# Kernel tuning notes

Measured on AMD Instinct MI355X. Metric: run time of the kernel, lower is better.

Reference implementation:

```python
import jax, jax.numpy as jnp
import numpy as np

WS = (8, 8)          # window_size
HEADS = 8
DH = 64              # dim_head
SHIFT = (4, 4)
SCALE = DH ** -0.5


def setup_inputs() -> dict:
    key = jax.random.key(0)
    ks = jax.random.split(key, 5)
    dim = 64
    inner = HEADS * DH  # 512
    b, h, w = 4, 192, 192
    x = jax.random.normal(ks[0], (b, h, w, dim), dtype=jnp.float32)
    Wq = jax.random.normal(ks[1], (dim, inner), dtype=jnp.float32) * (dim ** -0.5)
    Wkv = jax.random.normal(ks[2], (dim, 2 * inner), dtype=jnp.float32) * (dim ** -0.5)
    Wo = jax.random.normal(ks[3], (inner, dim), dtype=jnp.float32) * (inner ** -0.5)
    bo = jnp.zeros((dim,), dtype=jnp.float32)
    seq_l = WS[0] * WS[1]
    pos_emb = jax.random.normal(ks[4], (1, HEADS, seq_l, seq_l), dtype=jnp.float32)
    return {"x": x, "Wq": Wq, "Wkv": Wkv, "Wo": Wo, "bo": bo, "pos_emb": pos_emb}


def reference(x, Wq, Wkv, Wo, bo, pos_emb):
    b, h, w, c = x.shape
    L = WS[0] * WS[1]  # 64 tokens per window
    if SHIFT[0] > 0:
        x = jnp.roll(x, shift=(-SHIFT[0], -SHIFT[1]), axis=(1, 2))
    # NOTE: original uses a raw .view() here (row-major reshape), NOT an 8x8
    # window partition. Replicate exactly.
    nw = b * (h // WS[0]) * (w // WS[1])
    x_inp = x.reshape(nw, L, c)                      # [nw, 64, c]
    q = x_inp @ Wq                                   # [nw, 64, inner]
    kv = x_inp @ Wkv
    k, v = jnp.split(kv, 2, axis=-1)
    # original: raw view (nw, L, inner) -> (nw, heads, L, dh) (not a transpose)
    q = q.reshape(nw, HEADS, L, DH) * SCALE
    k = k.reshape(nw, HEADS, L, DH)
    v = v.reshape(nw, HEADS, L, DH)
    sim = jnp.einsum('bhid,bhjd->bhij', q, k) + pos_emb
    attn = jax.nn.softmax(sim, axis=-1)
    out = jnp.einsum('bhij,bhjd->bhid', attn, v)     # [nw, heads, 64, dh]
    # original: raw view back to (nw, L, inner)
    out = out.reshape(nw, L, HEADS * DH)
    out = out @ Wo + bo                              # [nw, 64, c]
    out = out.reshape(b, h, w, c)
    if SHIFT[0] > 0:
        out = jnp.roll(out, shift=(SHIFT[0], SHIFT[1]), axis=(1, 2))
    return out
```

## Files before the change

### kernel.cpp

```cpp
#include <hip/hip_runtime.h>
#include <stdint.h>

typedef __attribute__((ext_vector_type(8))) short bf16x8;
typedef __attribute__((ext_vector_type(4))) short s16x4;
typedef __attribute__((ext_vector_type(4))) float f32x4;

#define THREADS 256
constexpr int NWIN = 2304;

constexpr int WCATT_E = 0;
constexpr int WOT_E   = 98304;
constexpr int POS_E   = 131072;
constexpr size_t WS_NEED = 327680;

__device__ __forceinline__ short f2bf(float f) {
  uint32_t u = __builtin_bit_cast(uint32_t, f);
  u += 0x7fffu + ((u >> 16) & 1u);
  return (short)(u >> 16);
}
__device__ __forceinline__ float bf2f(short s) {
  uint32_t u = ((uint32_t)(uint16_t)s) << 16;
  return __builtin_bit_cast(float, u);
}
__device__ __forceinline__ int swz(int row, int h) {
  return ((((row ^ (row >> 2) ^ (row >> 3)) & 7) ^ h) << 4);
}

__global__ void wmsa_prep(const float* __restrict__ Wq, const float* __restrict__ Wkv,
                          const float* __restrict__ Wo, const float* __restrict__ pos,
                          short* __restrict__ ws) {
  int idx = blockIdx.x * 256 + threadIdx.x;
  if (idx < 32768) {
    int n = idx & 511, k = idx >> 9;
    ws[WCATT_E + n * 64 + k] = f2bf(Wq[k * 512 + n] * 0.125f);
  } else if (idx < 98304) {
    int j = idx - 32768;
    int nkv = j & 1023, k = j >> 10;
    ws[WCATT_E + (512 + nkv) * 64 + k] = f2bf(Wkv[k * 1024 + nkv]);
  } else if (idx < 131072) {
    int j = idx - 98304;
    int n = j & 63, k = j >> 6;
    ws[WOT_E + n * 512 + k] = f2bf(Wo[k * 64 + n]);
  } else if (idx < 163840) {
    int j = idx - 131072;
    ws[POS_E + j] = f2bf(pos[j]);
  }
}

__global__ __launch_bounds__(THREADS, 2)
void wmsa_mfma(const float* __restrict__ x, const float* __restrict__ bo,
               const short* __restrict__ ws, float* __restrict__ out) {
  __shared__ __align__(16) char lds[65536];
  const int tid = threadIdx.x;
  const int wv = tid >> 6;
  const int l  = tid & 63;
  const int lr = l & 15;
  const int lg = l >> 4;

  const int bid = blockIdx.x;
  const int p   = bid >> 2;
  const int hp  = bid & 3;

  const float* xrow[2];
  float* orow[2];
  int ww0a[2];
  #pragma unroll
  for (int win = 0; win < 2; ++win) {
    int w   = 2 * p + win;
    int t0  = w * 64;
    int bb  = t0 / 36864;
    int rem = t0 % 36864;
    int hh  = rem / 192;
    ww0a[win] = rem % 192;
    int src_h = (hh + 4) % 192;
    xrow[win] = x + (size_t)(bb * 192 + src_h) * 12288;
    orow[win] = out + (size_t)(bb * 192 + src_h) * 12288;
  }

  bf16x8 xa[2][2];
  #pragma unroll
  for (int win = 0; win < 2; ++win) {
    int tok = 16 * hp + lr;
    int sw = ww0a[win] + tok + 4; if (sw >= 192) sw -= 192;
    const float* xp = xrow[win] + sw * 64;
    #pragma unroll
    for (int ks = 0; ks < 2; ++ks) {
      float4 a = *(const float4*)(xp + ks * 32 + lg * 8);
      float4 b = *(const float4*)(xp + ks * 32 + lg * 8 + 4);
      bf16x8 v;
      v[0] = f2bf(a.x); v[1] = f2bf(a.y); v[2] = f2bf(a.z); v[3] = f2bf(a.w);
      v[4] = f2bf(b.x); v[5] = f2bf(b.y); v[6] = f2bf(b.z); v[7] = f2bf(b.w);
      xa[win][ks] = v;
    }
  }

  #pragma unroll 4
  for (int t = 0; t < 16; ++t) {
    int nt = wv + 4 * t;
    int nload = nt * 16 + lr;
    bf16x8 b0 = *(const bf16x8*)(ws + WCATT_E + nload * 64 + lg * 8);
    bf16x8 b1 = *(const bf16x8*)(ws + WCATT_E + nload * 64 + 32 + lg * 8);
    const bool isQ = (t < 8);
    int i  = (lr & 7) * 8 + (t & 7);
    int h2 = lr >> 3;
    int d0 = wv * 16 + lg * 4;
    int off = (isQ ? 0 : 16384) + h2 * 8192 + i * 128 + ((d0 * 2) ^ swz(i, h2));
    #pragma unroll
    for (int win = 0; win < 2; ++win) {
      f32x4 acc = {0.f, 0.f, 0.f, 0.f};
      acc = __builtin_amdgcn_mfma_f32_16x16x32_bf16(b0, xa[win][0], acc, 0, 0, 0);
      acc = __builtin_amdgcn_mfma_f32_16x16x32_bf16(b1, xa[win][1], acc, 0, 0, 0);
      s16x4 pk;
      #pragma unroll
      for (int r = 0; r < 4; ++r) pk[r] = f2bf(acc[r]);
      *(s16x4*)(lds + win * 32768 + off) = pk;
    }
  }

  f32x4 vacc[2][8];
  #pragma unroll
  for (int tv = 0; tv < 8; ++tv) {
    int nload = (64 + wv + 4 * tv) * 16 + lr;
    bf16x8 b0 = *(const bf16x8*)(ws + WCATT_E + nload * 64 + lg * 8);
    bf16x8 b1 = *(const bf16x8*)(ws + WCATT_E + nload * 64 + 32 + lg * 8);
    #pragma unroll
    for (int win = 0; win < 2; ++win) {
      f32x4 acc = {0.f, 0.f, 0.f, 0.f};
      acc = __builtin_amdgcn_mfma_f32_16x16x32_bf16(xa[win][0], b0, acc, 0, 0, 0);
      acc = __builtin_amdgcn_mfma_f32_16x16x32_bf16(xa[win][1], b1, acc, 0, 0, 0);
      vacc[win][tv] = acc;
    }
  }
  __syncthreads();

  const int hl = wv >> 1;
  const int ih = wv & 1;
  const int hglob = 2 * hp + hl;

  s16x4 posr[2][4];
  #pragma unroll
  for (int it = 0; it < 2; ++it) {
    int i = (ih * 2 + it) * 16 + lr;
    const short* pp = ws + POS_E + hglob * 4096 + i * 64;
    #pragma unroll
    for (int jt = 0; jt < 4; ++jt)
      posr[it][jt] = *(const s16x4*)(pp + jt * 16 + lg * 4);
  }

  #pragma unroll
  for (int win = 0; win < 2; ++win) {
    char* ldw = lds + win * 32768;
    f32x4 s[2][4];
    #pragma unroll
    for (int it = 0; it < 2; ++it)
      #pragma unroll
      for (int jt = 0; jt < 4; ++jt) s[it][jt] = (f32x4){0.f, 0.f, 0.f, 0.f};

    #pragma unroll
    for (int ks = 0; ks < 2; ++ks) {
      bf16x8 kb[4], qa[2];
      #pragma unroll
      for (int jt = 0; jt < 4; ++jt) {
        int j = jt * 16 + lr;
        kb[jt] = *(const bf16x8*)(ldw + 16384 + hl * 8192 + j * 128 + ((ks * 64 + lg * 16) ^ swz(j, hl)));
      }
      #pragma unroll
      for (int it = 0; it < 2; ++it) {
        int i = (ih * 2 + it) * 16 + lr;
        qa[it] = *(const bf16x8*)(ldw + hl * 8192 + i * 128 + ((ks * 64 + lg * 16) ^ swz(i, hl)));
      }
      __builtin_amdgcn_s_setprio(1);
      #pragma unroll
      for (int it = 0; it < 2; ++it)
        #pragma unroll
        for (int jt = 0; jt < 4; ++jt)
          s[it][jt] = __builtin_amdgcn_mfma_f32_16x16x32_bf16(kb[jt], qa[it], s[it][jt], 0, 0, 0);
      __builtin_amdgcn_s_setprio(0);
    }

    #pragma unroll
    for (int it = 0; it < 2; ++it) {
      int i = (ih * 2 + it) * 16 + lr;
      float sum = 0.f;
      #pragma unroll
      for (int jt = 0; jt < 4; ++jt)
        #pragma unroll
        for (int r = 0; r < 4; ++r) {
          float pv = __expf(s[it][jt][r] + bf2f(posr[it][jt][r]));
          s[it][jt][r] = pv;
          sum += pv;
        }
      sum += __shfl_xor(sum, 16);
      sum += __shfl_xor(sum, 32);
      float rinv = 1.f / sum;
      #pragma unroll
      for (int jt = 0; jt < 4; ++jt) {
        s16x4 pk;
        #pragma unroll
        for (int r = 0; r < 4; ++r) pk[r] = f2bf(s[it][jt][r] * rinv);
        *(s16x4*)(ldw + hl * 8192 + i * 128 + ((jt * 32 + lg * 8) ^ swz(i, hl))) = pk;
      }
    }
  }
  __syncthreads();

  {
    int d = wv * 16 + lr;
    #pragma unroll
    for (int win = 0; win < 2; ++win)
      #pragma unroll
      for (int r = 0; r < 4; ++r) {
        int tl = lg * 4 + r;
        int h2 = tl >> 3;
        int slot = tl & 7;
        bf16x8 pk;
        #pragma unroll
        for (int tv = 0; tv < 8; ++tv) pk[tv] = f2bf(vacc[win][tv][r]);
        *(bf16x8*)(lds + win * 32768 + 16384 + h2 * 8192 + d * 128 + ((slot * 16) ^ swz(d, h2))) = pk;
      }
  }
  __syncthreads();

  bf16x8 wofr[16];
  #pragma unroll
  for (int ks = 0; ks < 16; ++ks)
    wofr[ks] = *(const bf16x8*)(ws + WOT_E + (wv * 16 + lr) * 512 + ks * 32 + lg * 8);

  #pragma unroll
  for (int win = 0; win < 2; ++win) {
    char* ldw = lds + win * 32768;
    f32x4 o[2][4];
    #pragma unroll
    for (int it = 0; it < 2; ++it)
      #pragma unroll
      for (int dt = 0; dt < 4; ++dt) o[it][dt] = (f32x4){0.f, 0.f, 0.f, 0.f};
    #pragma unroll
    for (int ks = 0; ks < 2; ++ks) {
      bf16x8 vb[4], pa[2];
      #pragma unroll
      for (int dt = 0; dt < 4; ++dt) {
        int d = dt * 16 + lr;
        vb[dt] = *(const bf16x8*)(ldw + 16384 + hl * 8192 + d * 128 + ((ks * 64 + lg * 16) ^ swz(d, hl)));
      }
      #pragma unroll
      for (int it = 0; it < 2; ++it) {
        int i = (ih * 2 + it) * 16 + lr;
        pa[it] = *(const bf16x8*)(ldw + hl * 8192 + i * 128 + ((ks * 64 + lg * 16) ^ swz(i, hl)));
      }
      __builtin_amdgcn_s_setprio(1);
      #pragma unroll
      for (int it = 0; it < 2; ++it)
        #pragma unroll
        for (int dt = 0; dt < 4; ++dt)
          o[it][dt] = __builtin_amdgcn_mfma_f32_16x16x32_bf16(vb[dt], pa[it], o[it][dt], 0, 0, 0);
      __builtin_amdgcn_s_setprio(0);
    }
    #pragma unroll
    for (int it = 0; it < 2; ++it) {
      int i  = (ih * 2 + it) * 16 + lr;
      int lm = 8 * hl + (i >> 3);
      int rp = lm * 8 + (i & 7);
      #pragma unroll
      for (int dt = 0; dt < 4; ++dt) {
        s16x4 pk;
        #pragma unroll
        for (int r = 0; r < 4; ++r) pk[r] = f2bf(o[it][dt][r]);
        *(s16x4*)(ldw + rp * 128 + ((dt * 32 + lg * 8) ^ swz(rp, 0))) = pk;
      }
    }
  }
  __syncthreads();

  f32x4 oacc[2];
  oacc[0] = (f32x4){0.f, 0.f, 0.f, 0.f};
  oacc[1] = (f32x4){0.f, 0.f, 0.f, 0.f};
  #pragma unroll
  for (int ks = 0; ks < 16; ++ks) {
    int rp = lr * 8 + (ks >> 1);
    int boff = rp * 128 + (((ks & 1) * 64 + lg * 16) ^ swz(rp, 0));
    #pragma unroll
    for (int win = 0; win < 2; ++win) {
      bf16x8 bfrOH = *(const bf16x8*)(lds + win * 32768 + boff);
      oacc[win] = __builtin_amdgcn_mfma_f32_16x16x32_bf16(wofr[ks], bfrOH, oacc[win], 0, 0, 0);
    }
  }
  {
    int c0 = wv * 16 + lg * 4;
    float4 bo4 = *(const float4*)(bo + c0);
    int tok = 16 * hp + lr;
    #pragma unroll
    for (int win = 0; win < 2; ++win) {
      int sw = ww0a[win] + tok + 4; if (sw >= 192) sw -= 192;
      float4 ov;
      ov.x = oacc[win][0] + bo4.x; ov.y = oacc[win][1] + bo4.y;
      ov.z = oacc[win][2] + bo4.z; ov.w = oacc[win][3] + bo4.w;
      *(float4*)(orow[win] + sw * 64 + c0) = ov;
    }
  }
}

constexpr float SCALEF = 0.125f;
constexpr int XSo = 0, Q8V = 4096, KT = 8256, SIMB = 12608, REDM = 16960, REDS = 17216, SMEMF = 17472;
__device__ __forceinline__ float f4c(const float4& v, int k) {
  return k == 0 ? v.x : k == 1 ? v.y : k == 2 ? v.z : v.w;
}
__global__ __launch_bounds__(THREADS, 2)
void wmsa_fp32(const float* __restrict__ x, const float* __restrict__ Wq,
               const float* __restrict__ Wkv, const float* __restrict__ Wo,
               const float* __restrict__ bo, const float* __restrict__ pos,
               float* __restrict__ out) {
  __shared__ float sm[SMEMF];
  const int tid = threadIdx.x;
  const int w   = blockIdx.x;
  const int t0  = w * 64;
  const int bb  = t0 / 36864;
  const int rem = t0 % 36864;
  const int hh  = rem / 192;
  const int ww0 = rem % 192;
  const int src_h = (hh + 4) % 192;
  const float* xrow = x + (size_t)(bb * 192 + src_h) * 12288;
  float* orow = out + (size_t)(bb * 192 + src_h) * 12288;
  for (int u = tid; u < 1024; u += THREADS) {
    int tok = u >> 4, c4 = (u & 15) << 2;
    int sw = ww0 + tok + 4; if (sw >= 192) sw -= 192;
    *reinterpret_cast<float4*>(&sm[XSo + tok * 64 + c4]) =
        *reinterpret_cast<const float4*>(xrow + sw * 64 + c4);
  }
  __syncthreads();
  for (int h = 0; h < 8; ++h) {
    const float* xsrow = &sm[XSo + (8 * h) * 64];
    {
      float acc[4][8];
      for (int m = 0; m < 4; ++m) for (int r = 0; r < 8; ++r) acc[m][r] = 0.f;
      #pragma unroll 4
      for (int c = 0; c < 64; ++c) {
        float xv[8];
        #pragma unroll
        for (int r = 0; r < 8; ++r) xv[r] = xsrow[r * 64 + c];
        #pragma unroll
        for (int m = 0; m < 4; ++m) {
          int jg = tid + 256 * m;
          float wv = (m < 2) ? Wq[c * 512 + jg] : Wkv[c * 1024 + (jg - 512)];
          #pragma unroll
          for (int r = 0; r < 8; ++r) acc[m][r] += xv[r] * wv;
        }
      }
      for (int m = 0; m < 2; ++m) { int qc = tid + 256 * m;
        for (int r = 0; r < 8; ++r) sm[Q8V + r * 520 + qc] = acc[m][r] * SCALEF; }
      for (int m = 2; m < 4; ++m) { int kc = tid + 256 * m - 512;
        int d = kc & 63, jh = kc >> 6;
        for (int r = 0; r < 8; ++r) sm[KT + d * 68 + 8 * r + jh] = acc[m][r]; }
    }
    __syncthreads();
    const int i0 = (tid >> 4) << 2;
    const int j0 = (tid & 15) << 2;
    {
      float s4[4][4];
      for (int a = 0; a < 4; ++a) for (int b = 0; b < 4; ++b) s4[a][b] = 0.f;
      #pragma unroll 2
      for (int dc = 0; dc < 64; dc += 4) {
        float4 q4[4], k4[4];
        #pragma unroll
        for (int a = 0; a < 4; ++a) { int i = i0 + a;
          q4[a] = *reinterpret_cast<const float4*>(&sm[Q8V + (i >> 3) * 520 + ((i & 7) << 6) + dc]); }
        #pragma unroll
        for (int dd = 0; dd < 4; ++dd)
          k4[dd] = *reinterpret_cast<const float4*>(&sm[KT + (dc + dd) * 68 + j0]);
        #pragma unroll
        for (int a = 0; a < 4; ++a)
          #pragma unroll
          for (int dd = 0; dd < 4; ++dd) {
            float qv = f4c(q4[a], dd);
            s4[a][0] += qv * k4[dd].x; s4[a][1] += qv * k4[dd].y;
            s4[a][2] += qv * k4[dd].z; s4[a][3] += qv * k4[dd].w;
          }
      }
      #pragma unroll
      for (int a = 0; a < 4; ++a) {
        float4 pv = *reinterpret_cast<const float4*>(&pos[((h * 64 + i0 + a) << 6) + j0]);
        float4 oo;
        oo.x = s4[a][0] + pv.x; oo.y = s4[a][1] + pv.y;
        oo.z = s4[a][2] + pv.z; oo.w = s4[a][3] + pv.w;
        *reinterpret_cast<float4*>(&sm[SIMB + (i0 + a) * 68 + j0]) = oo;
      }
    }
    __syncthreads();
    {
      float va[2][8];
      for (int m = 0; m < 2; ++m) for (int r = 0; r < 8; ++r) va[m][r] = 0.f;
      #pragma unroll 4
      for (int c = 0; c < 64; ++c) {
        float xv[8];
        #pragma unroll
        for (int r = 0; r < 8; ++r) xv[r] = xsrow[r * 64 + c];
        #pragma unroll
        for (int m = 0; m < 2; ++m) {
          float wv = Wkv[c * 1024 + 512 + tid + 256 * m];
          #pragma unroll
          for (int r = 0; r < 8; ++r) va[m][r] += xv[r] * wv;
        }
      }
      for (int m = 0; m < 2; ++m) { int vc = tid + 256 * m;
        for (int r = 0; r < 8; ++r) sm[Q8V + r * 520 + vc] = va[m][r]; }
    }
    {
      const int i = tid & 63, seg = tid >> 6;
      float* srow = &sm[SIMB + i * 68 + seg * 16];
      float mloc = -1e30f;
      #pragma unroll
      for (int u = 0; u < 16; ++u) mloc = fmaxf(mloc, srow[u]);
      sm[REDM + i * 4 + seg] = mloc;
      __syncthreads();
      float mrow = fmaxf(fmaxf(sm[REDM + i * 4 + 0], sm[REDM + i * 4 + 1]),
                         fmaxf(sm[REDM + i * 4 + 2], sm[REDM + i * 4 + 3]));
      float ssum = 0.f;
      #pragma unroll
      for (int u = 0; u < 16; ++u) {
        float p = __expf(srow[u] - mrow); srow[u] = p; ssum += p;
      }
      sm[REDS + i * 4 + seg] = ssum;
    }
    __syncthreads();
    {
      float rinv[4];
      #pragma unroll
      for (int a = 0; a < 4; ++a) {
        const float* rs = &sm[REDS + (i0 + a) * 4];
        rinv[a] = 1.f / (rs[0] + rs[1] + rs[2] + rs[3]);
      }
      float o4[4][4];
      for (int a = 0; a < 4; ++a) for (int b = 0; b < 4; ++b) o4[a][b] = 0.f;
      #pragma unroll 2
      for (int j = 0; j < 64; ++j) {
        float4 v4 = *reinterpret_cast<const float4*>(&sm[Q8V + (j >> 3) * 520 + ((j & 7) << 6) + j0]);
        #pragma unroll
        for (int a = 0; a < 4; ++a) {
          float p = sm[SIMB + (i0 + a) * 68 + j];
          o4[a][0] += p * v4.x; o4[a][1] += p * v4.y;
          o4[a][2] += p * v4.z; o4[a][3] += p * v4.w;
        }
      }
      __syncthreads();
      #pragma unroll
      for (int a = 0; a < 4; ++a) {
        float4 oo;
        oo.x = o4[a][0] * rinv[a]; oo.y = o4[a][1] * rinv[a];
        oo.z = o4[a][2] * rinv[a]; oo.w = o4[a][3] * rinv[a];
        *reinterpret_cast<float4*>(&sm[KT + (i0 + a) * 64 + j0]) = oo;
      }
    }
    __syncthreads();
    {
      const int c = tid & 63;
      const int r2 = tid >> 6;
      float acc0 = bo[c], acc1 = bo[c];
      const float* ohp = &sm[KT];
      #pragma unroll 8
      for (int jj = 0; jj < 512; ++jj) {
        float wv = Wo[jj * 64 + c];
        int jh = jj >> 6, dd = jj & 63;
        acc0 += ohp[(8 * r2 + jh) * 64 + dd] * wv;
        acc1 += ohp[(8 * (r2 + 4) + jh) * 64 + dd] * wv;
      }
      int l0 = 8 * h + r2, l1 = l0 + 4;
      int sw0 = ww0 + l0 + 4; if (sw0 >= 192) sw0 -= 192;
      int sw1 = ww0 + l1 + 4; if (sw1 >= 192) sw1 -= 192;
      orow[(size_t)sw0 * 64 + c] = acc0;
      orow[(size_t)sw1 * 64 + c] = acc1;
    }
    __syncthreads();
  }
}

extern "C" void kernel_launch(void* const* d_in, const int* in_sizes, int n_in,
                              void* d_out, int out_size, void* d_ws, size_t ws_size,
                              hipStream_t stream) {
  const float* x    = (const float*)d_in[0];
  const float* Wq   = (const float*)d_in[1];
  const float* Wkv  = (const float*)d_in[2];
  const float* Wo   = (const float*)d_in[3];
  const float* bo   = (const float*)d_in[4];
  const float* pos  = (const float*)d_in[5];
  float* o = (float*)d_out;
  if (ws_size >= WS_NEED) {
    wmsa_prep<<<dim3(640), dim3(256), 0, stream>>>(Wq, Wkv, Wo, pos, (short*)d_ws);
    wmsa_mfma<<<dim3(NWIN * 2), dim3(THREADS), 0, stream>>>(x, bo, (const short*)d_ws, o);
  } else {
    wmsa_fp32<<<dim3(NWIN), dim3(THREADS), 0, stream>>>(x, Wq, Wkv, Wo, bo, pos, o);
  }
}
```

Measured before the change: 185.8 us.

## Add 512-thread kernel processing four windows per block with shared weight fragments

Introduces a new MFMA kernel where each 512-thread block handles four windows for one token quarter, reusing each QKV and output-projection weight fragment across four windows. It uses 128KB of dynamic LDS and keeps V projections in registers until the softmax phase finishes. The softmax drops max subtraction, which risks overflow. The larger LDS footprint may reduce occupancy. The fp32 fallback kernel is removed.

```diff
diff --git a/kernel.cpp b/kernel.cpp
--- a/kernel.cpp
+++ b/kernel.cpp
@@ -47,6 +47,258 @@
   }
 }
 
+__global__ __launch_bounds__(512, 2)
+void wmsa_mfma4(const float* __restrict__ x, const float* __restrict__ bo,
+                const short* __restrict__ ws, float* __restrict__ out) {
+  extern __shared__ __align__(16) char lds[];
+  const int tid = threadIdx.x;
+  const int wv = tid >> 6;
+  const int l  = tid & 63;
+  const int lr = l & 15;
+  const int lg = l >> 4;
+
+  const int bid = blockIdx.x;
+  const int q   = bid >> 2;
+  const int hp  = bid & 3;
+
+  bf16x8 xa[4][2];
+  #pragma unroll
+  for (int win = 0; win < 4; ++win) {
+    int w   = 4 * q + win;
+    int bb  = w / 576;
+    int rem = (w * 64) % 36864;
+    int hh  = rem / 192;
+    int ww0 = rem % 192;
+    int src_h = (hh + 4) % 192;
+    const float* xp = x + (size_t)(bb * 192 + src_h) * 12288;
+    int tok = 16 * hp + lr;
+    int sw = ww0 + tok + 4; if (sw >= 192) sw -= 192;
+    const float* xq = xp + sw * 64;
+    #pragma unroll
+    for (int ks = 0; ks < 2; ++ks) {
+      float4 a = *(const float4*)(xq + ks * 32 + lg * 8);
+      float4 b = *(const float4*)(xq + ks * 32 + lg * 8 + 4);
+      bf16x8 v;
+      v[0] = f2bf(a.x); v[1] = f2bf(a.y); v[2] = f2bf(a.z); v[3] = f2bf(a.w);
+      v[4] = f2bf(b.x); v[5] = f2bf(b.y); v[6] = f2bf(b.z); v[7] = f2bf(b.w);
+      xa[win][ks] = v;
+    }
+  }
+
+  #pragma unroll
+  for (int t = 0; t < 8; ++t) {
+    int nt = wv + 8 * t;
+    int nload = nt * 16 + lr;
+    bf16x8 b0 = *(const bf16x8*)(ws + WCATT_E + nload * 64 + lg * 8);
+    bf16x8 b1 = *(const bf16x8*)(ws + WCATT_E + nload * 64 + 32 + lg * 8);
+    const bool isQ = (t < 4);
+    int i  = (lr & 7) * 8 + ((nt >> 2) & 7);
+    int h2 = lr >> 3;
+    int d0 = (nt & 3) * 16 + lg * 4;
+    int off = (isQ ? 0 : 16384) + h2 * 8192 + i * 128 + ((d0 * 2) ^ swz(i, h2));
+    #pragma unroll
+    for (int win = 0; win < 4; ++win) {
+      f32x4 acc = {0.f, 0.f, 0.f, 0.f};
+      acc = __builtin_amdgcn_mfma_f32_16x16x32_bf16(b0, xa[win][0], acc, 0, 0, 0);
+      acc = __builtin_amdgcn_mfma_f32_16x16x32_bf16(b1, xa[win][1], acc, 0, 0, 0);
+      s16x4 pk;
+      #pragma unroll
+      for (int r = 0; r < 4; ++r) pk[r] = f2bf(acc[r]);
+      *(s16x4*)(lds + win * 32768 + off) = pk;
+    }
+  }
+
+  const int bq = wv & 3, aq = wv >> 2;
+  f32x4 vacc[4][4];
+  #pragma unroll
+  for (int u = 0; u < 4; ++u) {
+    int ntile = (aq * 4 + u) * 4 + bq;
+    int nload = (64 + ntile) * 16 + lr;
+    bf16x8 b0 = *(const bf16x8*)(ws + WCATT_E + nload * 64 + lg * 8);
+    bf16x8 b1 = *(const bf16x8*)(ws + WCATT_E + nload * 64 + 32 + lg * 8);
+    #pragma unroll
+    for (int win = 0; win < 4; ++win) {
+      f32x4 acc = {0.f, 0.f, 0.f, 0.f};
+      acc = __builtin_amdgcn_mfma_f32_16x16x32_bf16(xa[win][0], b0, acc, 0, 0, 0);
+      acc = __builtin_amdgcn_mfma_f32_16x16x32_bf16(xa[win][1], b1, acc, 0, 0, 0);
+      vacc[win][u] = acc;
+    }
+  }
+  __syncthreads();
+
+  const int hl = (wv >> 1) & 1;
+  const int ih = wv & 1;
+  const int hglob = 2 * hp + hl;
+  const int wbase = aq;
+
+  s16x4 posr[2][4];
+  #pragma unroll
+  for (int it = 0; it < 2; ++it) {
+    int i = (ih * 2 + it) * 16 + lr;
+    const short* pp = ws + POS_E + hglob * 4096 + i * 64;
+    #pragma unroll
+    for (int jt = 0; jt < 4; ++jt)
+      posr[it][jt] = *(const s16x4*)(pp + jt * 16 + lg * 4);
+  }
+
+  #pragma unroll
+  for (int c = 0; c < 2; ++c) {
+    char* ldw = lds + (wbase + 2 * c) * 32768;
+    f32x4 s[2][4];
+    #pragma unroll
+    for (int it = 0; it < 2; ++it)
+      #pragma unroll
+      for (int jt = 0; jt < 4; ++jt) s[it][jt] = (f32x4){0.f, 0.f, 0.f, 0.f};
+
+    #pragma unroll
+    for (int ks = 0; ks < 2; ++ks) {
+      bf16x8 kb[4], qa[2];
+      #pragma unroll
+      for (int jt = 0; jt < 4; ++jt) {
+        int j = jt * 16 + lr;
+        kb[jt] = *(const bf16x8*)(ldw + 16384 + hl * 8192 + j * 128 + ((ks * 64 + lg * 16) ^ swz(j, hl)));
+      }
+      #pragma unroll
+      for (int it = 0; it < 2; ++it) {
+        int i = (ih * 2 + it) * 16 + lr;
+        qa[it] = *(const bf16x8*)(ldw + hl * 8192 + i * 128 + ((ks * 64 + lg * 16) ^ swz(i, hl)));
+      }
+      __builtin_amdgcn_s_setprio(1);
+      #pragma unroll
+      for (int it = 0; it < 2; ++it)
+        #pragma unroll
+        for (int jt = 0; jt < 4; ++jt)
+          s[it][jt] = __builtin_amdgcn_mfma_f32_16x16x32_bf16(kb[jt], qa[it], s[it][jt], 0, 0, 0);
+      __builtin_amdgcn_s_setprio(0);
+    }
+
+    #pragma unroll
+    for (int it = 0; it < 2; ++it) {
+      int i = (ih * 2 + it) * 16 + lr;
+      float sum = 0.f;
+      #pragma unroll
+      for (int jt = 0; jt < 4; ++jt)
+        #pragma unroll
+        for (int r = 0; r < 4; ++r) {
+          float pv = __expf(s[it][jt][r] + bf2f(posr[it][jt][r]));
+          s[it][jt][r] = pv;
+          sum += pv;
+        }
+      sum += __shfl_xor(sum, 16);
+      sum += __shfl_xor(sum, 32);
+      float rinv = 1.f / sum;
+      #pragma unroll
+      for (int jt = 0; jt < 4; ++jt) {
+        s16x4 pk;
+        #pragma unroll
+        for (int r = 0; r < 4; ++r) pk[r] = f2bf(s[it][jt][r] * rinv);
+        *(s16x4*)(ldw + hl * 8192 + i * 128 + ((jt * 32 + lg * 8) ^ swz(i, hl))) = pk;
+      }
+    }
+  }
+  __syncthreads();
+
+  {
+    int d = bq * 16 + lr;
+    #pragma unroll
+    for (int win = 0; win < 4; ++win)
+      #pragma unroll
+      for (int r = 0; r < 4; ++r) {
+        int tl = lg * 4 + r;
+        int h2 = tl >> 3;
+        int jb = (tl & 7) * 16 + aq * 8;
+        s16x4 pk;
+        #pragma unroll
+        for (int u = 0; u < 4; ++u) pk[u] = f2bf(vacc[win][u][r]);
+        *(s16x4*)(lds + win * 32768 + 16384 + h2 * 8192 + d * 128 + (jb ^ swz(d, h2))) = pk;
+      }
+  }
+  __syncthreads();
+
+  bf16x8 wofr[16];
+  #pragma unroll
+  for (int ks = 0; ks < 16; ++ks)
+    wofr[ks] = *(const bf16x8*)(ws + WOT_E + (bq * 16 + lr) * 512 + ks * 32 + lg * 8);
+
+  #pragma unroll
+  for (int c = 0; c < 2; ++c) {
+    char* ldw = lds + (wbase + 2 * c) * 32768;
+    f32x4 o[2][4];
+    #pragma unroll
+    for (int it = 0; it < 2; ++it)
+      #pragma unroll
+      for (int dt = 0; dt < 4; ++dt) o[it][dt] = (f32x4){0.f, 0.f, 0.f, 0.f};
+    #pragma unroll
+    for (int ks = 0; ks < 2; ++ks) {
+      bf16x8 vb[4], pa[2];
+      #pragma unroll
+      for (int dt = 0; dt < 4; ++dt) {
+        int d = dt * 16 + lr;
+        vb[dt] = *(const bf16x8*)(ldw + 16384 + hl * 8192 + d * 128 + ((ks * 64 + lg * 16) ^ swz(d, hl)));
+      }
+      #pragma unroll
+      for (int it = 0; it < 2; ++it) {
+        int i = (ih * 2 + it) * 16 + lr;
+        pa[it] = *(const bf16x8*)(ldw + hl * 8192 + i * 128 + ((ks * 64 + lg * 16) ^ swz(i, hl)));
+      }
+      __builtin_amdgcn_s_setprio(1);
+      #pragma unroll
+      for (int it = 0; it < 2; ++it)
+        #pragma unroll
+        for (int dt = 0; dt < 4; ++dt)
+          o[it][dt] = __builtin_amdgcn_mfma_f32_16x16x32_bf16(vb[dt], pa[it], o[it][dt], 0, 0, 0);
+      __builtin_amdgcn_s_setprio(0);
+    }
+    #pragma unroll
+    for (int it = 0; it < 2; ++it) {
+      int i  = (ih * 2 + it) * 16 + lr;
+      int lm = 8 * hl + (i >> 3);
+      int rp = lm * 8 + (i & 7);
+      #pragma unroll
+      for (int dt = 0; dt < 4; ++dt) {
+        s16x4 pk;
+        #pragma unroll
+        for (int r = 0; r < 4; ++r) pk[r] = f2bf(o[it][dt][r]);
+        *(s16x4*)(ldw + rp * 128 + ((dt * 32 + lg * 8) ^ swz(rp, 0))) = pk;
+      }
+    }
+  }
+  __syncthreads();
+
+  f32x4 oacc0 = {0.f, 0.f, 0.f, 0.f};
+  f32x4 oacc1 = {0.f, 0.f, 0.f, 0.f};
+  #pragma unroll
+  for (int ks = 0; ks < 16; ++ks) {
+    int rp = lr * 8 + (ks >> 1);
+    int boff = rp * 128 + (((ks & 1) * 64 + lg * 16) ^ swz(rp, 0));
+    bf16x8 bA = *(const bf16x8*)(lds + wbase * 32768 + boff);
+    bf16x8 bB = *(const bf16x8*)(lds + (wbase + 2) * 32768 + boff);
+    oacc0 = __builtin_amdgcn_mfma_f32_16x16x32_bf16(wofr[ks], bA, oacc0, 0, 0, 0);
+    oacc1 = __builtin_amdgcn_mfma_f32_16x16x32_bf16(wofr[ks], bB, oacc1, 0, 0, 0);
+  }
+  {
+    int c0 = bq * 16 + lg * 4;
+    float4 bo4 = *(const float4*)(bo + c0);
+    int tok = 16 * hp + lr;
+    #pragma unroll
+    for (int c = 0; c < 2; ++c) {
+      int w   = 4 * q + wbase + 2 * c;
+      int bb  = w / 576;
+      int rem = (w * 64) % 36864;
+      int hh  = rem / 192;
+      int ww0 = rem % 192;
+      int src_h = (hh + 4) % 192;
+      float* orow = out + (size_t)(bb * 192 + src_h) * 12288;
+      int sw = ww0 + tok + 4; if (sw >= 192) sw -= 192;
+      f32x4 oa = c ? oacc1 : oacc0;
+      float4 ov;
+      ov.x = oa[0] + bo4.x; ov.y = oa[1] + bo4.y;
+      ov.z = oa[2] + bo4.z; ov.w = oa[3] + bo4.w;
+      *(float4*)(orow + sw * 64 + c0) = ov;
+    }
+  }
+}
+
 __global__ __launch_bounds__(THREADS, 2)
 void wmsa_mfma(const float* __restrict__ x, const float* __restrict__ bo,
                const short* __restrict__ ws, float* __restrict__ out) {
@@ -296,179 +548,6 @@
       ov.z = oacc[win][2] + bo4.z; ov.w = oacc[win][3] + bo4.w;
       *(float4*)(orow[win] + sw * 64 + c0) = ov;
     }
-  }
-}
-
-constexpr float SCALEF = 0.125f;
-constexpr int XSo = 0, Q8V = 4096, KT = 8256, SIMB = 12608, REDM = 16960, REDS = 17216, SMEMF = 17472;
-__device__ __forceinline__ float f4c(const float4& v, int k) {
-  return k == 0 ? v.x : k == 1 ? v.y : k == 2 ? v.z : v.w;
-}
-__global__ __launch_bounds__(THREADS, 2)
-void wmsa_fp32(const float* __restrict__ x, const float* __restrict__ Wq,
-               const float* __restrict__ Wkv, const float* __restrict__ Wo,
-               const float* __restrict__ bo, const float* __restrict__ pos,
-               float* __restrict__ out) {
-  __shared__ float sm[SMEMF];
-  const int tid = threadIdx.x;
-  const int w   = blockIdx.x;
-  const int t0  = w * 64;
-  const int bb  = t0 / 36864;
-  const int rem = t0 % 36864;
-  const int hh  = rem / 192;
-  const int ww0 = rem % 192;
-  const int src_h = (hh + 4) % 192;
-  const float* xrow = x + (size_t)(bb * 192 + src_h) * 12288;
-  float* orow = out + (size_t)(bb * 192 + src_h) * 12288;
-  for (int u = tid; u < 1024; u += THREADS) {
-    int tok = u >> 4, c4 = (u & 15) << 2;
-    int sw = ww0 + tok + 4; if (sw >= 192) sw -= 192;
-    *reinterpret_cast<float4*>(&sm[XSo + tok * 64 + c4]) =
-        *reinterpret_cast<const float4*>(xrow + sw * 64 + c4);
-  }
-  __syncthreads();
-  for (int h = 0; h < 8; ++h) {
-    const float* xsrow = &sm[XSo + (8 * h) * 64];
-    {
-      float acc[4][8];
-      for (int m = 0; m < 4; ++m) for (int r = 0; r < 8; ++r) acc[m][r] = 0.f;
-      #pragma unroll 4
-      for (int c = 0; c < 64; ++c) {
-        float xv[8];
-        #pragma unroll
-        for (int r = 0; r < 8; ++r) xv[r] = xsrow[r * 64 + c];
-        #pragma unroll
-        for (int m = 0; m < 4; ++m) {
-          int jg = tid + 256 * m;
-          float wv = (m < 2) ? Wq[c * 512 + jg] : Wkv[c * 1024 + (jg - 512)];
-          #pragma unroll
-          for (int r = 0; r < 8; ++r) acc[m][r] += xv[r] * wv;
-        }
-      }
-      for (int m = 0; m < 2; ++m) { int qc = tid + 256 * m;
-        for (int r = 0; r < 8; ++r) sm[Q8V + r * 520 + qc] = acc[m][r] * SCALEF; }
-      for (int m = 2; m < 4; ++m) { int kc = tid + 256 * m - 512;
-        int d = kc & 63, jh = kc >> 6;
-        for (int r = 0; r < 8; ++r) sm[KT + d * 68 + 8 * r + jh] = acc[m][r]; }
-    }
-    __syncthreads();
-    const int i0 = (tid >> 4) << 2;
-    const int j0 = (tid & 15) << 2;
-    {
-      float s4[4][4];
-      for (int a = 0; a < 4; ++a) for (int b = 0; b < 4; ++b) s4[a][b] = 0.f;
-      #pragma unroll 2
-      for (int dc = 0; dc < 64; dc += 4) {
-        float4 q4[4], k4[4];
-        #pragma unroll
-        for (int a = 0; a < 4; ++a) { int i = i0 + a;
-          q4[a] = *reinterpret_cast<const float4*>(&sm[Q8V + (i >> 3) * 520 + ((i & 7) << 6) + dc]); }
-        #pragma unroll
-        for (int dd = 0; dd < 4; ++dd)
-          k4[dd] = *reinterpret_cast<const float4*>(&sm[KT + (dc + dd) * 68 + j0]);
-        #pragma unroll
-        for (int a = 0; a < 4; ++a)
-          #pragma unroll
-          for (int dd = 0; dd < 4; ++dd) {
-            float qv = f4c(q4[a], dd);
-            s4[a][0] += qv * k4[dd].x; s4[a][1] += qv * k4[dd].y;
-            s4[a][2] += qv * k4[dd].z; s4[a][3] += qv * k4[dd].w;
-          }
-      }
-      #pragma unroll
-      for (int a = 0; a < 4; ++a) {
-        float4 pv = *reinterpret_cast<const float4*>(&pos[((h * 64 + i0 + a) << 6) + j0]);
-        float4 oo;
-        oo.x = s4[a][0] + pv.x; oo.y = s4[a][1] + pv.y;
-        oo.z = s4[a][2] + pv.z; oo.w = s4[a][3] + pv.w;
-        *reinterpret_cast<float4*>(&sm[SIMB + (i0 + a) * 68 + j0]) = oo;
-      }
-    }
-    __syncthreads();
-    {
-      float va[2][8];
-      for (int m = 0; m < 2; ++m) for (int r = 0; r < 8; ++r) va[m][r] = 0.f;
-      #pragma unroll 4
-      for (int c = 0; c < 64; ++c) {
-        float xv[8];
-        #pragma unroll
-        for (int r = 0; r < 8; ++r) xv[r] = xsrow[r * 64 + c];
-        #pragma unroll
-        for (int m = 0; m < 2; ++m) {
-          float wv = Wkv[c * 1024 + 512 + tid + 256 * m];
-          #pragma unroll
-          for (int r = 0; r < 8; ++r) va[m][r] += xv[r] * wv;
-        }
-      }
-      for (int m = 0; m < 2; ++m) { int vc = tid + 256 * m;
-        for (int r = 0; r < 8; ++r) sm[Q8V + r * 520 + vc] = va[m][r]; }
-    }
-    {
-      const int i = tid & 63, seg = tid >> 6;
-      float* srow = &sm[SIMB + i * 68 + seg * 16];
-      float mloc = -1e30f;
-      #pragma unroll
-      for (int u = 0; u < 16; ++u) mloc = fmaxf(mloc, srow[u]);
-      sm[REDM + i * 4 + seg] = mloc;
-      __syncthreads();
-      float mrow = fmaxf(fmaxf(sm[REDM + i * 4 + 0], sm[REDM + i * 4 + 1]),
-                         fmaxf(sm[REDM + i * 4 + 2], sm[REDM + i * 4 + 3]));
-      float ssum = 0.f;
-      #pragma unroll
-      for (int u = 0; u < 16; ++u) {
-        float p = __expf(srow[u] - mrow); srow[u] = p; ssum += p;
-      }
-      sm[REDS + i * 4 + seg] = ssum;
-    }
-    __syncthreads();
-    {
-      float rinv[4];
-      #pragma unroll
-      for (int a = 0; a < 4; ++a) {
-        const float* rs = &sm[REDS + (i0 + a) * 4];
-        rinv[a] = 1.f / (rs[0] + rs[1] + rs[2] + rs[3]);
-      }
-      float o4[4][4];
-      for (int a = 0; a < 4; ++a) for (int b = 0; b < 4; ++b) o4[a][b] = 0.f;
-      #pragma unroll 2
-      for (int j = 0; j < 64; ++j) {
-        float4 v4 = *reinterpret_cast<const float4*>(&sm[Q8V + (j >> 3) * 520 + ((j & 7) << 6) + j0]);
-        #pragma unroll
-        for (int a = 0; a < 4; ++a) {
-          float p = sm[SIMB + (i0 + a) * 68 + j];
-          o4[a][0] += p * v4.x; o4[a][1] += p * v4.y;
-          o4[a][2] += p * v4.z; o4[a][3] += p * v4.w;
-        }
-      }
-      __syncthreads();
-      #pragma unroll
-      for (int a = 0; a < 4; ++a) {
-        float4 oo;
-        oo.x = o4[a][0] * rinv[a]; oo.y = o4[a][1] * rinv[a];
-        oo.z = o4[a][2] * rinv[a]; oo.w = o4[a][3] * rinv[a];
-        *reinterpret_cast<float4*>(&sm[KT + (i0 + a) * 64 + j0]) = oo;
-      }
-    }
-    __syncthreads();
-    {
-      const int c = tid & 63;
-      const int r2 = tid >> 6;
-      float acc0 = bo[c], acc1 = bo[c];
-      const float* ohp = &sm[KT];
-      #pragma unroll 8
-      for (int jj = 0; jj < 512; ++jj) {
-        float wv = Wo[jj * 64 + c];
-        int jh = jj >> 6, dd = jj & 63;
-        acc0 += ohp[(8 * r2 + jh) * 64 + dd] * wv;
-        acc1 += ohp[(8 * (r2 + 4) + jh) * 64 + dd] * wv;
-      }
-      int l0 = 8 * h + r2, l1 = l0 + 4;
-      int sw0 = ww0 + l0 + 4; if (sw0 >= 192) sw0 -= 192;
-      int sw1 = ww0 + l1 + 4; if (sw1 >= 192) sw1 -= 192;
-      orow[(size_t)sw0 * 64 + c] = acc0;
-      orow[(size_t)sw1 * 64 + c] = acc1;
-    }
-    __syncthreads();
   }
 }
 
@@ -484,8 +563,15 @@
   float* o = (float*)d_out;
   if (ws_size >= WS_NEED) {
     wmsa_prep<<<dim3(640), dim3(256), 0, stream>>>(Wq, Wkv, Wo, pos, (short*)d_ws);
+    hipError_t e = hipFuncSetAttribute((const void*)wmsa_mfma4,
+                                       hipFuncAttributeMaxDynamicSharedMemorySize, 131072);
+    if (e == hipSuccess) {
+      wmsa_mfma4<<<dim3(NWIN), dim3(512), 131072, stream>>>(x, bo, (const short*)d_ws, o);
+    } else {
+      wmsa_mfma<<<dim3(NWIN * 2), dim3(THREADS), 0, stream>>>(x, bo, (const short*)d_ws, o);
+    }
+  } else {
+    wmsa_prep<<<dim3(640), dim3(256), 0, stream>>>(Wq, Wkv, Wo, pos, (short*)d_ws);
     wmsa_mfma<<<dim3(NWIN * 2), dim3(THREADS), 0, stream>>>(x, bo, (const short*)d_ws, o);
-  } else {
-    wmsa_fp32<<<dim3(NWIN), dim3(THREADS), 0, stream>>>(x, Wq, Wkv, Wo, bo, pos, o);
-  }
-}
+  }
+}
```

Result: faster. 179.8 us (-3.2%).
